# Kernel optimization log

Measured on AMD Instinct MI355X. Metric: run time of the kernel, lower is better.

## Reference

```python
import jax, jax.numpy as jnp
from jax import lax
import numpy as np

LAM = 0.95          # config.agent.return_lambda
HORIZON = 333.0     # config.agent.horizon
# slowtar=True, contdisc=False

B, T, D, H = 1024, 16, 5120, 1024


def _mlp(feat, w1, b1, w2, b2, w3, b3):
    # critic MLP -> scalar mean per (b, t); [B,T,D] -> [B,T]
    h = jax.nn.silu(jnp.einsum('btd,dh->bth', feat, w1) + b1)
    h = jax.nn.silu(jnp.einsum('bth,hk->btk', h, w2) + b2)
    return jnp.einsum('bth,h->bt', h, w3) + b3[0]


def setup_inputs() -> dict:
    key = jax.random.key(0)
    ks = jax.random.split(key, 10)
    sc1 = 1.0 / np.sqrt(D)
    sc2 = 1.0 / np.sqrt(H)
    return {
        'feat': jax.random.normal(ks[0], (B, T, D), jnp.float32),
        'rew': jax.random.normal(ks[1], (B, T), jnp.float32),
        'cont': jax.random.uniform(ks[2], (B, T), jnp.float32),
        'net_w1': jax.random.normal(ks[3], (D, H), jnp.float32) * sc1,
        'net_b1': jnp.zeros((H,), jnp.float32),
        'net_w2': jax.random.normal(ks[4], (H, H), jnp.float32) * sc2,
        'net_b2': jnp.zeros((H,), jnp.float32),
        'net_w3': jax.random.normal(ks[5], (H,), jnp.float32) * sc2,
        'net_b3': jnp.zeros((1,), jnp.float32),
        'slow_w1': jax.random.normal(ks[6], (D, H), jnp.float32) * sc1,
        'slow_b1': jnp.zeros((H,), jnp.float32),
        'slow_w2': jax.random.normal(ks[7], (H, H), jnp.float32) * sc2,
        'slow_b2': jnp.zeros((H,), jnp.float32),
        'slow_w3': jax.random.normal(ks[8], (H,), jnp.float32) * sc2,
        'slow_b3': jnp.zeros((1,), jnp.float32),
        'voffset': jax.random.normal(ks[9], (1,), jnp.float32),
        'vscale': jax.random.uniform(jax.random.fold_in(key, 99), (1,), jnp.float32, minval=0.5, maxval=1.5),
    }


def reference(feat, rew, cont, net_w1, net_b1, net_w2, net_b2, net_w3, net_b3,
              slow_w1, slow_b1, slow_w2, slow_b2, slow_w3, slow_b3, voffset, vscale):
    critic = _mlp(feat, net_w1, net_b1, net_w2, net_b2, net_w3, net_b3)        # [B,T]
    slowcritic = _mlp(feat, slow_w1, slow_b1, slow_w2, slow_b2, slow_w3, slow_b3)
    val = critic * vscale[0] + voffset[0]
    slowval = slowcritic * vscale[0] + voffset[0]
    tarval = slowval  # slowtar = True
    discount = 1.0 - 1.0 / HORIZON  # contdisc = False
    disc = cont[:, 1:] * discount                                 # [B,T-1]
    interm = rew[:, 1:] + (1.0 - LAM) * disc * tarval[:, 1:]      # [B,T-1]

    def step(carry, xs):
        i_t, d_t = xs
        r = i_t + d_t * LAM * carry
        return r, r

    # reversed linear recurrence over time: rets[t] = interm[t] + disc[t]*lam*rets[t+1]
    _, ys = lax.scan(step, tarval[:, -1], (interm.T, disc.T), reverse=True)  # [T-1,B]
    ret = ys.T                                                    # [B,T-1]
    return rew, ret, tarval, critic, slowcritic
```

## Files before the change

### kernel.cpp

```cpp
#include <hip/hip_runtime.h>
#include <stdint.h>

typedef unsigned short u16;
typedef __attribute__((ext_vector_type(8))) __bf16 bf16x8;
typedef __attribute__((ext_vector_type(8))) u16 u16x8;
typedef __attribute__((ext_vector_type(4))) u16 u16x4;
typedef __attribute__((ext_vector_type(4))) float f32x4;

#define LAM 0.95f
#define DISCOUNT (1.0f - 1.0f / 333.0f)

constexpr int Bsz = 1024, Tsz = 16, Dsz = 5120, Hsz = 1024;
constexpr int Msz = Bsz * Tsz;
constexpr int Nsz = 2 * Hsz;

__device__ __forceinline__ u16 f2bf(float x) {
  union { float f; uint32_t u; } un; un.f = x;
  uint32_t u = un.u;
  return (u16)((u + 0x7FFFu + ((u >> 16) & 1u)) >> 16);
}
__device__ __forceinline__ float bf2f(u16 u) {
  union { uint32_t u; float f; } un; un.u = ((uint32_t)u) << 16;
  return un.f;
}
__device__ __forceinline__ void async16(const void* g, void* l) {
  __builtin_amdgcn_global_load_lds(
      (const __attribute__((address_space(1))) uint32_t*)g,
      (__attribute__((address_space(3))) uint32_t*)l, 16, 0, 0);
}

__global__ __launch_bounds__(256) void transpose_cvt(
    const float* __restrict__ src, u16* __restrict__ dst, int K, int N) {
  __shared__ float tile[64][65];
  int k0 = blockIdx.x * 64, n0 = blockIdx.y * 64;
  int tid = threadIdx.x;
#pragma unroll
  for (int i = 0; i < 16; ++i) {
    int idx = i * 256 + tid, rr = idx >> 6, cc = idx & 63;
    tile[rr][cc] = src[(size_t)(k0 + rr) * N + n0 + cc];
  }
  __syncthreads();
#pragma unroll
  for (int i = 0; i < 16; ++i) {
    int idx = i * 256 + tid, rr = idx >> 6, cc = idx & 63;
    dst[(size_t)(n0 + rr) * K + k0 + cc] = f2bf(tile[cc][rr]);
  }
}

__global__ void prep_bias(const float* nb1, const float* sb1, const float* nb2,
                          const float* sb2, float* bias1, float* bias2) {
  int i = blockIdx.x * 256 + threadIdx.x;
  if (i < 1024) { bias1[i] = nb1[i]; bias2[i] = nb2[i]; }
  else if (i < 2048) { bias1[i] = sb1[i - 1024]; bias2[i] = sb2[i - 1024]; }
}

__global__ void cvt_f32_to_bf16(const float* __restrict__ src, u16* __restrict__ dst, int n4) {
  int i = blockIdx.x * 256 + threadIdx.x;
  int stride = gridDim.x * 256;
  for (; i < n4; i += stride) {
    float4 v = ((const float4*)src)[i];
    u16x4 o; o[0] = f2bf(v.x); o[1] = f2bf(v.y); o[2] = f2bf(v.z); o[3] = f2bf(v.w);
    ((u16x4*)dst)[i] = o;
  }
}

template <bool A_F32>
__global__ __launch_bounds__(256) void gemm_bias_silu(
    const void* __restrict__ Ap, const u16* __restrict__ Bp,
    const float* __restrict__ bias, u16* __restrict__ Out,
    int K, int lda, int a_half_off) {
  __shared__ u16 ldsA[128 * 64];
  __shared__ u16 ldsB[128 * 64];

  const int tid = threadIdx.x;
  const int lane = tid & 63;
  const int wv = tid >> 6;
  const int wm = (wv >> 1) << 6;
  const int wn = (wv & 1) << 6;
  const int lm = lane & 15, lq = lane >> 4, l7 = lane & 7;

  const int flat = blockIdx.x;
  const int grp = flat >> 8, r = flat & 255;
  const int m0 = (grp * 16 + (r & 15)) * 128;
  const int n0 = (r >> 4) * 128;
  const int a_off = (n0 >= (Nsz / 2)) ? a_half_off : 0;

  const u16* bsrc[4];
  const float* asrcf[4];
  const u16* asrcb[4];
  u16* ldsAd[4];
  u16* ldsBd[4];
#pragma unroll
  for (int i = 0; i < 4; ++i) {
    int cid = i * 256 + tid;
    int row = cid >> 3, ch = cid & 7;
    int kp = ch ^ (row & 7);
    bsrc[i] = Bp + (size_t)(n0 + row) * K + kp * 8;
    if (A_F32) asrcf[i] = (const float*)Ap + (size_t)(m0 + row) * lda + a_off + kp * 8;
    else       asrcb[i] = (const u16*)Ap + (size_t)(m0 + row) * lda + a_off + kp * 8;
    ldsAd[i] = &ldsA[cid * 8];
    ldsBd[i] = &ldsB[cid * 8];
  }

  int rA[4], rB[4];
#pragma unroll
  for (int t = 0; t < 4; ++t) {
    rA[t] = (wm + t * 16 + lm) * 64;
    rB[t] = (wn + t * 16 + lm) * 64;
  }

  f32x4 acc[4][4];
#pragma unroll
  for (int a = 0; a < 4; ++a)
#pragma unroll
    for (int b = 0; b < 4; ++b) acc[a][b] = f32x4{0.f, 0.f, 0.f, 0.f};

  for (int kt = 0; kt < K; kt += 64) {
#pragma unroll
    for (int i = 0; i < 4; ++i) async16(bsrc[i] + kt, ldsBd[i]);
    if (A_F32) {
      float4 v0[4], v1[4];
#pragma unroll
      for (int i = 0; i < 4; ++i) {
        const float* p = asrcf[i] + kt;
        v0[i] = *(const float4*)p;
        v1[i] = *(const float4*)(p + 4);
      }
#pragma unroll
      for (int i = 0; i < 4; ++i) {
        u16x8 pk;
        pk[0] = f2bf(v0[i].x); pk[1] = f2bf(v0[i].y); pk[2] = f2bf(v0[i].z); pk[3] = f2bf(v0[i].w);
        pk[4] = f2bf(v1[i].x); pk[5] = f2bf(v1[i].y); pk[6] = f2bf(v1[i].z); pk[7] = f2bf(v1[i].w);
        *(u16x8*)ldsAd[i] = pk;
      }
    } else {
#pragma unroll
      for (int i = 0; i < 4; ++i) async16(asrcb[i] + kt, ldsAd[i]);
    }
    __syncthreads();
#pragma unroll
    for (int ks = 0; ks < 2; ++ks) {
      const int ck = ((ks << 2) + lq) ^ l7;
      bf16x8 af[4], bfr[4];
#pragma unroll
      for (int t = 0; t < 4; ++t) af[t] = *(const bf16x8*)&ldsA[rA[t] + ck * 8];
#pragma unroll
      for (int t = 0; t < 4; ++t) bfr[t] = *(const bf16x8*)&ldsB[rB[t] + ck * 8];
#pragma unroll
      for (int a = 0; a < 4; ++a)
#pragma unroll
        for (int b = 0; b < 4; ++b)
          acc[a][b] = __builtin_amdgcn_mfma_f32_16x16x32_bf16(af[a], bfr[b], acc[a][b], 0, 0, 0);
    }
    __syncthreads();
  }

#pragma unroll
  for (int a = 0; a < 4; ++a) {
    int mrow = m0 + wm + a * 16 + lq * 4;
#pragma unroll
    for (int b = 0; b < 4; ++b) {
      int col = n0 + wn + b * 16 + lm;
      float bia = bias[col];
#pragma unroll
      for (int rr = 0; rr < 4; ++rr) {
        float v = acc[a][b][rr] + bia;
        v = v * (1.0f / (1.0f + __expf(-v)));
        Out[(size_t)(mrow + rr) * Nsz + col] = f2bf(v);
      }
    }
  }
}

__global__ __launch_bounds__(256) void head_k(
    const u16* __restrict__ h2, const float* __restrict__ nw3, const float* __restrict__ nb3,
    const float* __restrict__ sw3, const float* __restrict__ sb3,
    const float* __restrict__ voff, const float* __restrict__ vscl,
    float* __restrict__ critic, float* __restrict__ slow, float* __restrict__ tarv) {
  int lane = threadIdx.x & 63;
  int m = (blockIdx.x << 2) + (threadIdx.x >> 6);
  const u16* row = h2 + (size_t)m * Nsz;
  float sn = 0.f, ss = 0.f;
#pragma unroll
  for (int half = 0; half < 2; ++half) {
    const u16* base = row + half * 1024 + lane * 16;
    const float* w3 = (half ? sw3 : nw3) + lane * 16;
    u16x8 a0 = *(const u16x8*)base;
    u16x8 a1 = *(const u16x8*)(base + 8);
    float s = 0.f;
#pragma unroll
    for (int j = 0; j < 8; ++j) {
      s += bf2f(a0[j]) * w3[j];
      s += bf2f(a1[j]) * w3[8 + j];
    }
    if (half) ss = s; else sn = s;
  }
#pragma unroll
  for (int o = 32; o > 0; o >>= 1) {
    sn += __shfl_down(sn, o);
    ss += __shfl_down(ss, o);
  }
  if (lane == 0) {
    float c = sn + nb3[0];
    float sc = ss + sb3[0];
    critic[m] = c;
    slow[m] = sc;
    tarv[m] = sc * vscl[0] + voff[0];
  }
}

__global__ void scan_k(const float* __restrict__ rew, const float* __restrict__ cont,
                       const float* __restrict__ tarv, float* __restrict__ o_rew,
                       float* __restrict__ o_ret) {
  int b = blockIdx.x * 256 + threadIdx.x;
  if (b >= Bsz) return;
  float tv[Tsz], rw[Tsz];
#pragma unroll
  for (int t = 0; t < Tsz; ++t) {
    tv[t] = tarv[b * Tsz + t];
    rw[t] = rew[b * Tsz + t];
    o_rew[b * Tsz + t] = rw[t];
  }
  float carry = tv[Tsz - 1];
#pragma unroll
  for (int t = Tsz - 2; t >= 0; --t) {
    float d = cont[b * Tsz + t + 1] * DISCOUNT;
    float interm = rw[t + 1] + (1.0f - LAM) * d * tv[t + 1];
    carry = interm + d * LAM * carry;
    o_ret[b * (Tsz - 1) + t] = carry;
  }
}

constexpr size_t WT1_OFF = 0;
constexpr size_t WT1_BYTES = (size_t)Nsz * Dsz * 2;
constexpr size_t WT2_OFF = WT1_OFF + WT1_BYTES;
constexpr size_t WT2_BYTES = (size_t)Nsz * Hsz * 2;
constexpr size_t B1_OFF = WT2_OFF + WT2_BYTES;
constexpr size_t B2_OFF = B1_OFF + 8192;
constexpr size_t H1_OFF = B2_OFF + 8192;
constexpr size_t H_BYTES = (size_t)Msz * Nsz * 2;
constexpr size_t H2_OFF = H1_OFF + H_BYTES;
constexpr size_t FEATB_OFF = H2_OFF + H_BYTES;
constexpr size_t FEATB_BYTES = (size_t)Msz * Dsz * 2;
constexpr size_t NEED_BIG = FEATB_OFF + FEATB_BYTES;

extern "C" void kernel_launch(void* const* d_in, const int* in_sizes, int n_in,
                              void* d_out, int out_size, void* d_ws, size_t ws_size,
                              hipStream_t stream) {
  const float* feat = (const float*)d_in[0];
  const float* rew  = (const float*)d_in[1];
  const float* cont = (const float*)d_in[2];
  const float* nw1  = (const float*)d_in[3];
  const float* nb1  = (const float*)d_in[4];
  const float* nw2  = (const float*)d_in[5];
  const float* nb2  = (const float*)d_in[6];
  const float* nw3  = (const float*)d_in[7];
  const float* nb3  = (const float*)d_in[8];
  const float* sw1  = (const float*)d_in[9];
  const float* sb1  = (const float*)d_in[10];
  const float* sw2  = (const float*)d_in[11];
  const float* sb2  = (const float*)d_in[12];
  const float* sw3  = (const float*)d_in[13];
  const float* sb3  = (const float*)d_in[14];
  const float* voff = (const float*)d_in[15];
  const float* vscl = (const float*)d_in[16];

  char* ws = (char*)d_ws;
  u16* wt1 = (u16*)(ws + WT1_OFF);
  u16* wt2 = (u16*)(ws + WT2_OFF);
  float* bias1 = (float*)(ws + B1_OFF);
  float* bias2 = (float*)(ws + B2_OFF);
  u16* h1 = (u16*)(ws + H1_OFF);
  u16* h2 = (u16*)(ws + H2_OFF);
  u16* featb = (u16*)(ws + FEATB_OFF);
  const bool big = ws_size >= NEED_BIG;

  float* out = (float*)d_out;
  float* o_rew = out;
  float* o_ret = out + 16384;
  float* o_tar = out + 31744;
  float* o_cri = out + 48128;
  float* o_slo = out + 64512;

  transpose_cvt<<<dim3(Dsz / 64, Hsz / 64), 256, 0, stream>>>(nw1, wt1, Dsz, Hsz);
  transpose_cvt<<<dim3(Dsz / 64, Hsz / 64), 256, 0, stream>>>(sw1, wt1 + (size_t)Hsz * Dsz, Dsz, Hsz);
  transpose_cvt<<<dim3(Hsz / 64, Hsz / 64), 256, 0, stream>>>(nw2, wt2, Hsz, Hsz);
  transpose_cvt<<<dim3(Hsz / 64, Hsz / 64), 256, 0, stream>>>(sw2, wt2 + (size_t)Hsz * Hsz, Hsz, Hsz);
  prep_bias<<<8, 256, 0, stream>>>(nb1, sb1, nb2, sb2, bias1, bias2);

  const int gemm_grid = (Msz / 128) * (Nsz / 128);
  if (big) {
    cvt_f32_to_bf16<<<4096, 256, 0, stream>>>(feat, featb, Msz * Dsz / 4);
    gemm_bias_silu<false><<<gemm_grid, 256, 0, stream>>>(featb, wt1, bias1, h1, Dsz, Dsz, 0);
  } else {
    gemm_bias_silu<true><<<gemm_grid, 256, 0, stream>>>(feat, wt1, bias1, h1, Dsz, Dsz, 0);
  }
  gemm_bias_silu<false><<<gemm_grid, 256, 0, stream>>>(h1, wt2, bias2, h2, Hsz, Nsz, Hsz);
  head_k<<<Msz / 4, 256, 0, stream>>>(h2, nw3, nb3, sw3, sb3, voff, vscl, o_cri, o_slo, o_tar);
  scan_k<<<4, 256, 0, stream>>>(rew, cont, o_tar, o_rew, o_ret);
}
```

Measured before the change: 1.106 ms.

## Fuse head dot-product into second GEMM epilogue and stage outputs via LDS

The second GEMM now computes the w3 head dot product in its epilogue and reduces it per row with shuffles and atomicAdd, so h2 is never written or re-read. The first GEMM stages its bf16 output through padded LDS for coalesced 16-byte stores, block-to-tile mapping is reworked for XCD locality, transposes are vectorized, and the scan is merged with finalize. Accumulators must be zeroed in a prep kernel, and the atomics make the summation order nondeterministic.

```diff
diff --git a/kernel.cpp b/kernel.cpp
--- a/kernel.cpp
+++ b/kernel.cpp
@@ -13,15 +13,12 @@
 constexpr int Bsz = 1024, Tsz = 16, Dsz = 5120, Hsz = 1024;
 constexpr int Msz = Bsz * Tsz;
 constexpr int Nsz = 2 * Hsz;
+constexpr int ES = 136;
 
 __device__ __forceinline__ u16 f2bf(float x) {
   union { float f; uint32_t u; } un; un.f = x;
   uint32_t u = un.u;
   return (u16)((u + 0x7FFFu + ((u >> 16) & 1u)) >> 16);
-}
-__device__ __forceinline__ float bf2f(u16 u) {
-  union { uint32_t u; float f; } un; un.u = ((uint32_t)u) << 16;
-  return un.f;
 }
 __device__ __forceinline__ void async16(const void* g, void* l) {
   __builtin_amdgcn_global_load_lds(
@@ -35,23 +32,31 @@
   int k0 = blockIdx.x * 64, n0 = blockIdx.y * 64;
   int tid = threadIdx.x;
 #pragma unroll
-  for (int i = 0; i < 16; ++i) {
-    int idx = i * 256 + tid, rr = idx >> 6, cc = idx & 63;
-    tile[rr][cc] = src[(size_t)(k0 + rr) * N + n0 + cc];
+  for (int i = 0; i < 4; ++i) {
+    int idx = i * 256 + tid, rr = idx >> 4, c4 = (idx & 15) * 4;
+    float4 v = *(const float4*)&src[(size_t)(k0 + rr) * N + n0 + c4];
+    tile[rr][c4 + 0] = v.x; tile[rr][c4 + 1] = v.y;
+    tile[rr][c4 + 2] = v.z; tile[rr][c4 + 3] = v.w;
   }
   __syncthreads();
 #pragma unroll
-  for (int i = 0; i < 16; ++i) {
-    int idx = i * 256 + tid, rr = idx >> 6, cc = idx & 63;
-    dst[(size_t)(n0 + rr) * K + k0 + cc] = f2bf(tile[cc][rr]);
-  }
-}
-
-__global__ void prep_bias(const float* nb1, const float* sb1, const float* nb2,
-                          const float* sb2, float* bias1, float* bias2) {
+  for (int i = 0; i < 4; ++i) {
+    int idx = i * 256 + tid, rr = idx >> 4, c4 = (idx & 15) * 4;
+    u16x4 o;
+    o[0] = f2bf(tile[c4 + 0][rr]); o[1] = f2bf(tile[c4 + 1][rr]);
+    o[2] = f2bf(tile[c4 + 2][rr]); o[3] = f2bf(tile[c4 + 3][rr]);
+    *(u16x4*)&dst[(size_t)(n0 + rr) * K + k0 + c4] = o;
+  }
+}
+
+__global__ void prep_small(const float* nb1, const float* sb1, const float* nb2,
+                           const float* sb2, const float* nw3, const float* sw3,
+                           float* bias1, float* bias2, float* w3cat,
+                           float* accN, float* accS) {
   int i = blockIdx.x * 256 + threadIdx.x;
-  if (i < 1024) { bias1[i] = nb1[i]; bias2[i] = nb2[i]; }
-  else if (i < 2048) { bias1[i] = sb1[i - 1024]; bias2[i] = sb2[i - 1024]; }
+  if (i < 1024) { bias1[i] = nb1[i]; bias2[i] = nb2[i]; w3cat[i] = nw3[i]; }
+  else if (i < 2048) { bias1[i] = sb1[i - 1024]; bias2[i] = sb2[i - 1024]; w3cat[i] = sw3[i - 1024]; }
+  for (int j = i; j < Msz; j += gridDim.x * 256) { accN[j] = 0.f; accS[j] = 0.f; }
 }
 
 __global__ void cvt_f32_to_bf16(const float* __restrict__ src, u16* __restrict__ dst, int n4) {
@@ -64,13 +69,15 @@
   }
 }
 
-template <bool A_F32>
-__global__ __launch_bounds__(256) void gemm_bias_silu(
+template <int MODE, bool A_F32>
+__global__ __launch_bounds__(256) void gemm_fused(
     const void* __restrict__ Ap, const u16* __restrict__ Bp,
     const float* __restrict__ bias, u16* __restrict__ Out,
+    const float* __restrict__ w3cat, float* __restrict__ accN, float* __restrict__ accS,
     int K, int lda, int a_half_off) {
-  __shared__ u16 ldsA[128 * 64];
-  __shared__ u16 ldsB[128 * 64];
+  __shared__ __align__(16) u16 smem[(MODE == 0) ? (128 * ES) : 16384];
+  u16* ldsA = smem;
+  u16* ldsB = smem + 8192;
 
   const int tid = threadIdx.x;
   const int lane = tid & 63;
@@ -79,11 +86,15 @@
   const int wn = (wv & 1) << 6;
   const int lm = lane & 15, lq = lane >> 4, l7 = lane & 7;
 
-  const int flat = blockIdx.x;
-  const int grp = flat >> 8, r = flat & 255;
-  const int m0 = (grp * 16 + (r & 15)) * 128;
-  const int n0 = (r >> 4) * 128;
-  const int a_off = (n0 >= (Nsz / 2)) ? a_half_off : 0;
+  const int blk = blockIdx.x;
+  const int xcd = blk & 7;
+  const int l = blk >> 3;
+  const int quad = l >> 6;
+  const int mi = l & 7, ni = (l >> 3) & 7;
+  const int mt = xcd * 16 + ((quad & 1) << 3) + mi;
+  const int nt = ((quad >> 1) << 3) + ni;
+  const int m0 = mt << 7, n0 = nt << 7;
+  const int a_off = (n0 >= Hsz) ? a_half_off : 0;
 
   const u16* bsrc[4];
   const float* asrcf[4];
@@ -150,84 +161,89 @@
       for (int a = 0; a < 4; ++a)
 #pragma unroll
         for (int b = 0; b < 4; ++b)
-          acc[a][b] = __builtin_amdgcn_mfma_f32_16x16x32_bf16(af[a], bfr[b], acc[a][b], 0, 0, 0);
+          acc[a][b] = __builtin_amdgcn_mfma_f32_16x16x32_bf16(bfr[b], af[a], acc[a][b], 0, 0, 0);
     }
     __syncthreads();
   }
 
-#pragma unroll
-  for (int a = 0; a < 4; ++a) {
-    int mrow = m0 + wm + a * 16 + lq * 4;
-#pragma unroll
-    for (int b = 0; b < 4; ++b) {
-      int col = n0 + wn + b * 16 + lm;
-      float bia = bias[col];
-#pragma unroll
-      for (int rr = 0; rr < 4; ++rr) {
-        float v = acc[a][b][rr] + bia;
-        v = v * (1.0f / (1.0f + __expf(-v)));
-        Out[(size_t)(mrow + rr) * Nsz + col] = f2bf(v);
+  if (MODE == 0) {
+#pragma unroll
+    for (int a = 0; a < 4; ++a) {
+      int ml = wm + a * 16 + lm;
+#pragma unroll
+      for (int b = 0; b < 4; ++b) {
+        int nb = wn + b * 16 + lq * 4;
+        u16x4 pk;
+#pragma unroll
+        for (int rr = 0; rr < 4; ++rr) {
+          float v = acc[a][b][rr] + bias[n0 + nb + rr];
+          v = v * (1.0f / (1.0f + __expf(-v)));
+          pk[rr] = f2bf(v);
+        }
+        *(u16x4*)&smem[ml * ES + nb] = pk;
       }
     }
-  }
-}
-
-__global__ __launch_bounds__(256) void head_k(
-    const u16* __restrict__ h2, const float* __restrict__ nw3, const float* __restrict__ nb3,
-    const float* __restrict__ sw3, const float* __restrict__ sb3,
-    const float* __restrict__ voff, const float* __restrict__ vscl,
-    float* __restrict__ critic, float* __restrict__ slow, float* __restrict__ tarv) {
-  int lane = threadIdx.x & 63;
-  int m = (blockIdx.x << 2) + (threadIdx.x >> 6);
-  const u16* row = h2 + (size_t)m * Nsz;
-  float sn = 0.f, ss = 0.f;
-#pragma unroll
-  for (int half = 0; half < 2; ++half) {
-    const u16* base = row + half * 1024 + lane * 16;
-    const float* w3 = (half ? sw3 : nw3) + lane * 16;
-    u16x8 a0 = *(const u16x8*)base;
-    u16x8 a1 = *(const u16x8*)(base + 8);
-    float s = 0.f;
-#pragma unroll
-    for (int j = 0; j < 8; ++j) {
-      s += bf2f(a0[j]) * w3[j];
-      s += bf2f(a1[j]) * w3[8 + j];
-    }
-    if (half) ss = s; else sn = s;
-  }
-#pragma unroll
-  for (int o = 32; o > 0; o >>= 1) {
-    sn += __shfl_down(sn, o);
-    ss += __shfl_down(ss, o);
-  }
-  if (lane == 0) {
-    float c = sn + nb3[0];
-    float sc = ss + sb3[0];
-    critic[m] = c;
-    slow[m] = sc;
-    tarv[m] = sc * vscl[0] + voff[0];
-  }
-}
-
-__global__ void scan_k(const float* __restrict__ rew, const float* __restrict__ cont,
-                       const float* __restrict__ tarv, float* __restrict__ o_rew,
-                       float* __restrict__ o_ret) {
-  int b = blockIdx.x * 256 + threadIdx.x;
-  if (b >= Bsz) return;
-  float tv[Tsz], rw[Tsz];
-#pragma unroll
-  for (int t = 0; t < Tsz; ++t) {
-    tv[t] = tarv[b * Tsz + t];
-    rw[t] = rew[b * Tsz + t];
-    o_rew[b * Tsz + t] = rw[t];
-  }
-  float carry = tv[Tsz - 1];
-#pragma unroll
-  for (int t = Tsz - 2; t >= 0; --t) {
-    float d = cont[b * Tsz + t + 1] * DISCOUNT;
-    float interm = rw[t + 1] + (1.0f - LAM) * d * tv[t + 1];
-    carry = interm + d * LAM * carry;
-    o_ret[b * (Tsz - 1) + t] = carry;
+    __syncthreads();
+#pragma unroll
+    for (int i = 0; i < 8; ++i) {
+      int r = i * 16 + (tid >> 4);
+      int c = (tid & 15) * 8;
+      u16x8 vv = *(const u16x8*)&smem[r * ES + c];
+      *(u16x8*)&Out[(size_t)(m0 + r) * Nsz + n0 + c] = vv;
+    }
+  } else {
+    float pr[4] = {0.f, 0.f, 0.f, 0.f};
+#pragma unroll
+    for (int a = 0; a < 4; ++a) {
+#pragma unroll
+      for (int b = 0; b < 4; ++b) {
+        int nb = n0 + wn + b * 16 + lq * 4;
+#pragma unroll
+        for (int rr = 0; rr < 4; ++rr) {
+          float v = acc[a][b][rr] + bias[nb + rr];
+          v = v * (1.0f / (1.0f + __expf(-v)));
+          pr[a] += v * w3cat[nb + rr];
+        }
+      }
+    }
+    float* accp = (n0 < Hsz) ? accN : accS;
+#pragma unroll
+    for (int a = 0; a < 4; ++a) {
+      pr[a] += __shfl_xor(pr[a], 16);
+      pr[a] += __shfl_xor(pr[a], 32);
+      if (lq == 0) atomicAdd(&accp[m0 + wm + a * 16 + lm], pr[a]);
+    }
+  }
+}
+
+__global__ void finalize_scan(const float* __restrict__ accN, const float* __restrict__ accS,
+                              const float* __restrict__ nb3, const float* __restrict__ sb3,
+                              const float* __restrict__ voff, const float* __restrict__ vscl,
+                              const float* __restrict__ rew, const float* __restrict__ cont,
+                              float* __restrict__ o_rew, float* __restrict__ o_ret,
+                              float* __restrict__ o_tar, float* __restrict__ o_cri,
+                              float* __restrict__ o_slo) {
+  __shared__ float star[Tsz], srew[Tsz], scont[Tsz];
+  int b = blockIdx.x;
+  int t = threadIdx.x;
+  if (t < Tsz) {
+    int m = b * Tsz + t;
+    float c = accN[m] + nb3[0];
+    float s = accS[m] + sb3[0];
+    float tv = s * vscl[0] + voff[0];
+    o_cri[m] = c; o_slo[m] = s; o_tar[m] = tv;
+    float rw = rew[m];
+    o_rew[m] = rw;
+    star[t] = tv; srew[t] = rw; scont[t] = cont[m];
+  }
+  __syncthreads();
+  if (t == 0) {
+    float carry = star[Tsz - 1];
+    for (int k = Tsz - 2; k >= 0; --k) {
+      float d = scont[k + 1] * DISCOUNT;
+      carry = srew[k + 1] + (1.0f - LAM) * d * star[k + 1] + d * LAM * carry;
+      o_ret[b * (Tsz - 1) + k] = carry;
+    }
   }
 }
 
@@ -237,10 +253,12 @@
 constexpr size_t WT2_BYTES = (size_t)Nsz * Hsz * 2;
 constexpr size_t B1_OFF = WT2_OFF + WT2_BYTES;
 constexpr size_t B2_OFF = B1_OFF + 8192;
-constexpr size_t H1_OFF = B2_OFF + 8192;
+constexpr size_t W3_OFF = B2_OFF + 8192;
+constexpr size_t ACCN_OFF = W3_OFF + 8192;
+constexpr size_t ACCS_OFF = ACCN_OFF + (size_t)Msz * 4;
+constexpr size_t H1_OFF = ACCS_OFF + (size_t)Msz * 4;
 constexpr size_t H_BYTES = (size_t)Msz * Nsz * 2;
-constexpr size_t H2_OFF = H1_OFF + H_BYTES;
-constexpr size_t FEATB_OFF = H2_OFF + H_BYTES;
+constexpr size_t FEATB_OFF = H1_OFF + H_BYTES;
 constexpr size_t FEATB_BYTES = (size_t)Msz * Dsz * 2;
 constexpr size_t NEED_BIG = FEATB_OFF + FEATB_BYTES;
 
@@ -270,8 +288,10 @@
   u16* wt2 = (u16*)(ws + WT2_OFF);
   float* bias1 = (float*)(ws + B1_OFF);
   float* bias2 = (float*)(ws + B2_OFF);
+  float* w3cat = (float*)(ws + W3_OFF);
+  float* accN = (float*)(ws + ACCN_OFF);
+  float* accS = (float*)(ws + ACCS_OFF);
   u16* h1 = (u16*)(ws + H1_OFF);
-  u16* h2 = (u16*)(ws + H2_OFF);
   u16* featb = (u16*)(ws + FEATB_OFF);
   const bool big = ws_size >= NEED_BIG;
 
@@ -286,16 +306,19 @@
   transpose_cvt<<<dim3(Dsz / 64, Hsz / 64), 256, 0, stream>>>(sw1, wt1 + (size_t)Hsz * Dsz, Dsz, Hsz);
   transpose_cvt<<<dim3(Hsz / 64, Hsz / 64), 256, 0, stream>>>(nw2, wt2, Hsz, Hsz);
   transpose_cvt<<<dim3(Hsz / 64, Hsz / 64), 256, 0, stream>>>(sw2, wt2 + (size_t)Hsz * Hsz, Hsz, Hsz);
-  prep_bias<<<8, 256, 0, stream>>>(nb1, sb1, nb2, sb2, bias1, bias2);
+  prep_small<<<8, 256, 0, stream>>>(nb1, sb1, nb2, sb2, nw3, sw3, bias1, bias2, w3cat, accN, accS);
 
   const int gemm_grid = (Msz / 128) * (Nsz / 128);
   if (big) {
     cvt_f32_to_bf16<<<4096, 256, 0, stream>>>(feat, featb, Msz * Dsz / 4);
-    gemm_bias_silu<false><<<gemm_grid, 256, 0, stream>>>(featb, wt1, bias1, h1, Dsz, Dsz, 0);
+    gemm_fused<0, false><<<gemm_grid, 256, 0, stream>>>(
+        featb, wt1, bias1, h1, nullptr, nullptr, nullptr, Dsz, Dsz, 0);
   } else {
-    gemm_bias_silu<true><<<gemm_grid, 256, 0, stream>>>(feat, wt1, bias1, h1, Dsz, Dsz, 0);
-  }
-  gemm_bias_silu<false><<<gemm_grid, 256, 0, stream>>>(h1, wt2, bias2, h2, Hsz, Nsz, Hsz);
-  head_k<<<Msz / 4, 256, 0, stream>>>(h2, nw3, nb3, sw3, sb3, voff, vscl, o_cri, o_slo, o_tar);
-  scan_k<<<4, 256, 0, stream>>>(rew, cont, o_tar, o_rew, o_ret);
-}
+    gemm_fused<0, true><<<gemm_grid, 256, 0, stream>>>(
+        feat, wt1, bias1, h1, nullptr, nullptr, nullptr, Dsz, Dsz, 0);
+  }
+  gemm_fused<1, false><<<gemm_grid, 256, 0, stream>>>(
+      h1, wt2, bias2, nullptr, w3cat, accN, accS, Hsz, Nsz, Hsz);
+  finalize_scan<<<Bsz, 64, 0, stream>>>(accN, accS, nb3, sb3, voff, vscl, rew, cont,
+                                        o_rew, o_ret, o_tar, o_cri, o_slo);
+}
```

After: 1.043 ms. -5.7%, faster.
